# Kernel optimization log

Measured on AMD Instinct MI355X. Metric: run time of the kernel, lower is better.

Reference implementation:

```python
import math
import jax, jax.numpy as jnp
import numpy as np

LLM = 4096
QB = 512
SAM = 256
H = W = 64
OUT = 256
HEADS = 4
DH = SAM // HEADS
EPS = 1e-5


def _ln(x, g, b):
    mu = jnp.mean(x, axis=-1, keepdims=True)
    var = jnp.mean(jnp.square(x - mu), axis=-1, keepdims=True)
    return (x - mu) * jax.lax.rsqrt(var + EPS) * g + b


def _conv3x3(x, w):
    # x: (N,C,H,W), w: (O,I,3,3), padding=1
    return jax.lax.conv_general_dilated(
        x, w, window_strides=(1, 1), padding='SAME',
        dimension_numbers=('NCHW', 'OIHW', 'NCHW'))


def setup_inputs() -> dict:
    key = jax.random.key(0)
    ks = jax.random.split(key, 20)
    n = lambda k, sh, s: (jax.random.normal(k, sh, dtype=jnp.float32) * s)
    inp = {
        'image_embed': n(ks[0], (8, SAM, H, W), 1.0),
        'ref_vec': n(ks[1], (8, 32, LLM), 1.0),
        'querybook_slots': n(ks[2], (8, 32, QB), 1.0),
        # parameters (torch Linear layout: (out, in); conv: (O,I,kh,kw))
        'q_proj_w': n(ks[3], (HEADS * DH, LLM), 1.0 / math.sqrt(LLM)),
        'k_proj_w': n(ks[4], (HEADS * DH, SAM, 1, 1), 1.0 / math.sqrt(SAM)),
        'fuser_w1': n(ks[5], (HEADS, HEADS, 3, 3), 1.0 / math.sqrt(HEADS * 9)),
        'fuser_b1': n(ks[6], (HEADS,), 0.01),
        'fuser_w2': n(ks[7], (1, HEADS, 3, 3), 1.0 / math.sqrt(HEADS * 9)),
        'fuser_b2': jnp.full((1,), -1.8, dtype=jnp.float32),
        'qb_proj_w': n(ks[8], (LLM, QB), 1.0 / math.sqrt(QB)),
        'rf_ln_g': jnp.ones((2 * LLM,), jnp.float32),
        'rf_ln_b': jnp.zeros((2 * LLM,), jnp.float32),
        'rf_lin_w': n(ks[9], (LLM, 2 * LLM), 1.0 / math.sqrt(2 * LLM)),
        'rf_lin_b': n(ks[10], (LLM,), 0.01),
        'cf_ln_g': jnp.ones((LLM,), jnp.float32),
        'cf_ln_b': jnp.zeros((LLM,), jnp.float32),
        'cf_w1': n(ks[11], (LLM // 2, LLM), 1.0 / math.sqrt(LLM)),
        'cf_b1': n(ks[12], (LLM // 2,), 0.01),
        'cf_w2': n(ks[13], (1, LLM // 2), 1.0 / math.sqrt(LLM // 2)),
        'cf_b2': n(ks[14], (1,), 0.01),
    }
    return inp


def reference(image_embed, ref_vec, querybook_slots, q_proj_w, k_proj_w,
              fuser_w1, fuser_b1, fuser_w2, fuser_b2, qb_proj_w,
              rf_ln_g, rf_ln_b, rf_lin_w, rf_lin_b,
              cf_ln_g, cf_ln_b, cf_w1, cf_b1, cf_w2, cf_b2):
    B, C, h, w = image_embed.shape
    K = ref_vec.shape[1]
    # querybook projection + ref fuse
    qb = jnp.einsum('bkq,lq->bkl', querybook_slots, qb_proj_w)  # (B,K,LLM)
    cat = jnp.concatenate([ref_vec, qb], axis=-1)               # (B,K,2*LLM)
    fused = jax.nn.silu(jnp.einsum('bkc,lc->bkl', _ln(cat, rf_ln_g, rf_ln_b), rf_lin_w) + rf_lin_b)
    # per-slot query heads
    Q = jnp.einsum('bkl,ol->bko', fused, q_proj_w).reshape(B, K, HEADS, DH)
    # 1x1 conv key map -> (B,HEADS,DH,H,W)
    Kmap = jnp.einsum('bcxy,oc->boxy', image_embed, k_proj_w.reshape(HEADS * DH, SAM))
    Kmap = Kmap.reshape(B, HEADS, DH, h, w)
    # fused contraction over d_head (original materialized (B,K,HEADS,DH,H,W))
    logits_64_heads = jnp.einsum('bkhd,bhdxy->bkhxy', Q, Kmap) / math.sqrt(DH)
    x = logits_64_heads.reshape(B * K, HEADS, h, w)
    x = jax.nn.silu(_conv3x3(x, fuser_w1) + fuser_b1[None, :, None, None])
    logits_64 = _conv3x3(x, fuser_w2) + fuser_b2[None, :, None, None]  # (B*K,1,64,64)
    # bilinear upsample, align_corners=False (half-pixel centers)
    up = jax.image.resize(logits_64, (B * K, 1, OUT, OUT), method='bilinear')
    ref_logits_256 = up.reshape(B, K, OUT, OUT)
    # confidence head
    cfh = jax.nn.silu(jnp.einsum('bkl,ol->bko', _ln(fused, cf_ln_g, cf_ln_b), cf_w1) + cf_b1)
    conf_logits = (jnp.einsum('bko,lo->bkl', cfh, cf_w2) + cf_b2).squeeze(-1)  # (B,K)
    return ref_logits_256, conf_logits
```

## Files before the change

### kernel.cpp

```cpp
#include <hip/hip_runtime.h>

#define EPS 1e-5f

typedef __bf16 bf16_t;
typedef __bf16 bf16x8 __attribute__((ext_vector_type(8)));
typedef __bf16 bf16x4 __attribute__((ext_vector_type(4)));
typedef float f32x4 __attribute__((ext_vector_type(4)));

__device__ __forceinline__ float silu_f(float x) { return x / (1.f + __expf(-x)); }

__device__ __forceinline__ void gll16(const void* g, void* l) {
  __builtin_amdgcn_global_load_lds(
      (const __attribute__((address_space(1))) unsigned int*)g,
      (__attribute__((address_space(3))) unsigned int*)l, 16, 0, 0);
}

__device__ __forceinline__ float block_sum(float v, float* tmp) {
#pragma unroll
  for (int off = 32; off > 0; off >>= 1) v += __shfl_down(v, off);
  __syncthreads();
  if ((threadIdx.x & 63) == 0) tmp[threadIdx.x >> 6] = v;
  __syncthreads();
  return tmp[0] + tmp[1] + tmp[2] + tmp[3];
}

__global__ __launch_bounds__(1024) void gemm_gll(
    const bf16_t* __restrict__ A, const float* __restrict__ B,
    bf16_t* __restrict__ Cpart, int N, int K, int KS) {
  __shared__ bf16_t AsL[2][16384];
  __shared__ float BsL[2][8192];
  const int t = threadIdx.x;
  const int lane = t & 63;
  const int w = t >> 6;
  const int n0 = blockIdx.x * 128;
  const int kbeg = blockIdx.y * KS;
  const int nt = KS >> 6;

  const int arow0 = 16 * w + (lane >> 3);
  const int adch = (lane & 7) ^ (lane >> 3);
  const bf16_t* gA0 = A + (size_t)arow0 * K + kbeg + adch * 8;
  const bf16_t* gA1 = gA0 + (size_t)8 * K;
  const int brow0 = 8 * w + (lane >> 4);
  const int brow1 = brow0 + 4;
  const int bd0 = (lane & 15) ^ (brow0 & 15);
  const int bd1 = (lane & 15) ^ (brow1 & 15);
  const float* gB0 = B + (size_t)(n0 + brow0) * K + kbeg + bd0 * 4;
  const float* gB1 = B + (size_t)(n0 + brow1) * K + kbeg + bd1 * 4;

  f32x4 acc[4][2];
#pragma unroll
  for (int i = 0; i < 4; ++i)
#pragma unroll
    for (int j = 0; j < 2; ++j) acc[i][j] = f32x4{0.f, 0.f, 0.f, 0.f};

  const int wm = (w & 3) * 64;
  const int wn = (w >> 2) * 32;
  const int fr = lane & 15;
  const int kq = (lane >> 4) * 8;

  auto ISSUE = [&](int s, int p) {
    const int koff = s * 64;
    char* ab = (char*)&AsL[p][0] + 2 * w * 1024;
    char* bb = (char*)&BsL[p][0] + 2 * w * 1024;
    gll16(gA0 + koff, ab);
    gll16(gA1 + koff, ab + 1024);
    gll16(gB0 + koff, bb);
    gll16(gB1 + koff, bb + 1024);
  };

  auto COMPUTE = [&](int p) {
    const char* Ab = (const char*)&AsL[p][0];
    const char* Bb = (const char*)&BsL[p][0];
#pragma unroll
    for (int kk = 0; kk < 64; kk += 32) {
      const int col = kk + kq;
      bf16x8 af[4], bg[2];
#pragma unroll
      for (int i = 0; i < 4; ++i) {
        const int ra = wm + 16 * i + fr;
        const int sa = (col >> 3) ^ (ra & 7);
        af[i] = *(const bf16x8*)(Ab + ra * 128 + sa * 16);
      }
#pragma unroll
      for (int j = 0; j < 2; ++j) {
        const int rb = wn + 16 * j + fr;
        const int c0 = col >> 2;
        const int s0 = c0 ^ (rb & 15);
        const int s1 = (c0 + 1) ^ (rb & 15);
        f32x4 u0 = *(const f32x4*)(Bb + rb * 256 + s0 * 16);
        f32x4 u1 = *(const f32x4*)(Bb + rb * 256 + s1 * 16);
        bf16x8 bv;
        bv[0] = (bf16_t)u0[0]; bv[1] = (bf16_t)u0[1];
        bv[2] = (bf16_t)u0[2]; bv[3] = (bf16_t)u0[3];
        bv[4] = (bf16_t)u1[0]; bv[5] = (bf16_t)u1[1];
        bv[6] = (bf16_t)u1[2]; bv[7] = (bf16_t)u1[3];
        bg[j] = bv;
      }
#pragma unroll
      for (int i = 0; i < 4; ++i)
#pragma unroll
        for (int j = 0; j < 2; ++j)
          acc[i][j] = __builtin_amdgcn_mfma_f32_16x16x32_bf16(af[i], bg[j], acc[i][j], 0, 0, 0);
    }
  };

#define SB __builtin_amdgcn_sched_barrier(0);

  ISSUE(0, 0);
  if (nt > 1) ISSUE(1, 1);
  for (int s = 0; s < nt; ++s) {
    const int p = s & 1;
    if (s + 1 < nt) {
      asm volatile("s_waitcnt vmcnt(4)" ::: "memory");
    } else {
      asm volatile("s_waitcnt vmcnt(0)" ::: "memory");
    }
    SB __builtin_amdgcn_s_barrier(); SB
    COMPUTE(p);
    if (s + 2 < nt) {
      asm volatile("s_waitcnt lgkmcnt(0)" ::: "memory");
      SB __builtin_amdgcn_s_barrier(); SB
      ISSUE(s + 2, p);
    }
  }
#undef SB

  bf16_t* Cz = Cpart + (size_t)blockIdx.y * 256 * N;
  const int rh = (lane >> 4) * 4, col = lane & 15;
#pragma unroll
  for (int i = 0; i < 4; ++i)
#pragma unroll
    for (int j = 0; j < 2; ++j)
#pragma unroll
      for (int rr = 0; rr < 4; ++rr)
        Cz[(size_t)(wm + 16 * i + rh + rr) * N + n0 + wn + 16 * j + col] =
            (bf16_t)acc[i][j][rr];
}

__global__ __launch_bounds__(1024) void gemm_wide_s(
    const float* __restrict__ A, const float* __restrict__ B,
    bf16_t* __restrict__ Cpart, int N, int K, int KS) {
  __shared__ bf16_t As[256][72];
  __shared__ bf16_t Bs[128][72];
  const int t = threadIdx.x;
  const int lane = t & 63;
  const int w = t >> 6;
  const int n0 = blockIdx.x * 128;
  const int kbeg = blockIdx.y * KS;
  const int nt = KS >> 6;
  const int ar = t >> 2, ac = (t & 3) * 16;
  const int br = t >> 3, bc = (t & 7) * 8;
  const float* Ap = A + (size_t)ar * K + kbeg + ac;
  const float* Bp = B + (size_t)(n0 + br) * K + kbeg + bc;

  f32x4 acc[4][2];
#pragma unroll
  for (int i = 0; i < 4; ++i)
#pragma unroll
    for (int j = 0; j < 2; ++j) acc[i][j] = f32x4{0.f, 0.f, 0.f, 0.f};

  const int wm = (w & 3) * 64;
  const int wn = (w >> 2) * 32;
  const int fr = lane & 15;
  const int kq = (lane >> 4) * 8;

  for (int s = 0; s < nt; ++s) {
    float4 av[4], bv[2];
#pragma unroll
    for (int i = 0; i < 4; ++i) av[i] = *(const float4*)(Ap + s * 64 + 4 * i);
#pragma unroll
    for (int i = 0; i < 2; ++i) bv[i] = *(const float4*)(Bp + s * 64 + 4 * i);
    __syncthreads();
    {
      bf16x8 wa0, wa1, wb;
      wa0[0] = (bf16_t)av[0].x; wa0[1] = (bf16_t)av[0].y; wa0[2] = (bf16_t)av[0].z; wa0[3] = (bf16_t)av[0].w;
      wa0[4] = (bf16_t)av[1].x; wa0[5] = (bf16_t)av[1].y; wa0[6] = (bf16_t)av[1].z; wa0[7] = (bf16_t)av[1].w;
      wa1[0] = (bf16_t)av[2].x; wa1[1] = (bf16_t)av[2].y; wa1[2] = (bf16_t)av[2].z; wa1[3] = (bf16_t)av[2].w;
      wa1[4] = (bf16_t)av[3].x; wa1[5] = (bf16_t)av[3].y; wa1[6] = (bf16_t)av[3].z; wa1[7] = (bf16_t)av[3].w;
      wb[0] = (bf16_t)bv[0].x; wb[1] = (bf16_t)bv[0].y; wb[2] = (bf16_t)bv[0].z; wb[3] = (bf16_t)bv[0].w;
      wb[4] = (bf16_t)bv[1].x; wb[5] = (bf16_t)bv[1].y; wb[6] = (bf16_t)bv[1].z; wb[7] = (bf16_t)bv[1].w;
      *(bf16x8*)&As[ar][ac] = wa0;
      *(bf16x8*)&As[ar][ac + 8] = wa1;
      *(bf16x8*)&Bs[br][bc] = wb;
    }
    __syncthreads();
#pragma unroll
    for (int kk = 0; kk < 64; kk += 32) {
      bf16x8 af[4], bg[2];
#pragma unroll
      for (int i = 0; i < 4; ++i)
        af[i] = *(const bf16x8*)&As[wm + 16 * i + fr][kk + kq];
#pragma unroll
      for (int j = 0; j < 2; ++j)
        bg[j] = *(const bf16x8*)&Bs[wn + 16 * j + fr][kk + kq];
#pragma unroll
      for (int i = 0; i < 4; ++i)
#pragma unroll
        for (int j = 0; j < 2; ++j)
          acc[i][j] = __builtin_amdgcn_mfma_f32_16x16x32_bf16(af[i], bg[j], acc[i][j], 0, 0, 0);
    }
    __syncthreads();
  }

  bf16_t* Cz = Cpart + (size_t)blockIdx.y * 256 * N;
  const int rh = (lane >> 4) * 4, col = lane & 15;
#pragma unroll
  for (int i = 0; i < 4; ++i)
#pragma unroll
    for (int j = 0; j < 2; ++j)
#pragma unroll
      for (int rr = 0; rr < 4; ++rr)
        Cz[(size_t)(wm + 16 * i + rh + rr) * N + n0 + wn + 16 * j + col] =
            (bf16_t)acc[i][j][rr];
}

__global__ __launch_bounds__(256) void gemm_small(
    const bf16_t* __restrict__ A16, const float* __restrict__ B32, float* __restrict__ Cv,
    int M, int N, int K, int KS, int S) {
  __shared__ bf16_t As[64][72];
  __shared__ bf16_t Bs[64][72];
  const int t = threadIdx.x;
  const int lane = t & 63;
  const int w = t >> 6;
  const int s = blockIdx.z;
  const int n0 = blockIdx.x * 64;
  const int m0 = blockIdx.y * 64;
  const int kbeg = s * KS;

  f32x4 acc[2][2];
#pragma unroll
  for (int i = 0; i < 2; ++i)
#pragma unroll
    for (int j = 0; j < 2; ++j) acc[i][j] = f32x4{0.f, 0.f, 0.f, 0.f};

  const int wm = (w & 1) * 32, wn = (w >> 1) * 32;
  const int fr = lane & 15;
  const int kq = (lane >> 4) * 8;

  for (int k0 = kbeg; k0 < kbeg + KS; k0 += 64) {
    bf16x8 a8[2];
    float4 b4[4];
    {
      const int rr = t >> 2, c8 = (t & 3) * 8;
#pragma unroll
      for (int i = 0; i < 2; ++i)
        a8[i] = *(const bf16x8*)(A16 + (size_t)(m0 + rr) * K + k0 + c8 + 32 * i);
    }
    {
      const int rr = t >> 4, c4 = (t & 15) * 4;
#pragma unroll
      for (int i = 0; i < 4; ++i)
        b4[i] = *(const float4*)(B32 + (size_t)(n0 + rr + 16 * i) * K + k0 + c4);
    }
    __syncthreads();
    {
      const int rr = t >> 2, c8 = (t & 3) * 8;
#pragma unroll
      for (int i = 0; i < 2; ++i) *(bf16x8*)&As[rr][c8 + 32 * i] = a8[i];
    }
    {
      const int rr = t >> 4, c4 = (t & 15) * 4;
#pragma unroll
      for (int i = 0; i < 4; ++i) {
        bf16x4 v = {(bf16_t)b4[i].x, (bf16_t)b4[i].y, (bf16_t)b4[i].z, (bf16_t)b4[i].w};
        *(bf16x4*)&Bs[rr + 16 * i][c4] = v;
      }
    }
    __syncthreads();
#pragma unroll
    for (int kk = 0; kk < 64; kk += 32) {
      bf16x8 af[2], bg[2];
#pragma unroll
      for (int i = 0; i < 2; ++i) {
        af[i] = *(const bf16x8*)&As[wm + 16 * i + fr][kk + kq];
        bg[i] = *(const bf16x8*)&Bs[wn + 16 * i + fr][kk + kq];
      }
#pragma unroll
      for (int i = 0; i < 2; ++i)
#pragma unroll
        for (int j = 0; j < 2; ++j)
          acc[i][j] = __builtin_amdgcn_mfma_f32_16x16x32_bf16(af[i], bg[j], acc[i][j], 0, 0, 0);
    }
    __syncthreads();
  }

  const int rh = (lane >> 4) * 4;
  const int col = lane & 15;
#pragma unroll
  for (int i = 0; i < 2; ++i)
#pragma unroll
    for (int j = 0; j < 2; ++j)
#pragma unroll
      for (int rr = 0; rr < 4; ++rr)
        Cv[(size_t)s * M * N + (size_t)(m0 + wm + 16 * i + rh + rr) * N + n0 + wn + 16 * j + col] =
            acc[i][j][rr];
}

__global__ __launch_bounds__(512) void gemm_attn(
    const float* __restrict__ A, const float* __restrict__ B, bf16_t* __restrict__ C) {
  __shared__ bf16_t As[128][72];
  __shared__ bf16_t Bs[64][72];
  const int t = threadIdx.x;
  const int lane = t & 63;
  const int w = t >> 6;
  const int b = blockIdx.y;
  const int n0 = blockIdx.x * 64;
  const float* Ab = A + (size_t)b * 32768;
  const float* Bb = B + (size_t)b * 1048576;

  f32x4 acc[2][2];
#pragma unroll
  for (int i = 0; i < 2; ++i)
#pragma unroll
    for (int j = 0; j < 2; ++j) acc[i][j] = f32x4{0.f, 0.f, 0.f, 0.f};

  const int wm = (w & 3) * 32;
  const int wn = (w >> 2) * 32;
  const int fr = lane & 15;
  const int kq = (lane >> 4) * 8;

  for (int k0 = 0; k0 < 256; k0 += 64) {
    const int r = t >> 2, c4 = (t & 3) * 16;
    float4 a4[4];
#pragma unroll
    for (int i = 0; i < 4; ++i)
      a4[i] = *(const float4*)(Ab + (size_t)r * 256 + k0 + c4 + 4 * i);
    const int kr = t >> 3, nc = (t & 7) * 8;
    float4 b4[2];
#pragma unroll
    for (int i = 0; i < 2; ++i)
      b4[i] = *(const float4*)(Bb + (size_t)(k0 + kr) * 4096 + n0 + nc + 4 * i);
    __syncthreads();
#pragma unroll
    for (int i = 0; i < 4; ++i) {
      bf16x4 v = {(bf16_t)a4[i].x, (bf16_t)a4[i].y, (bf16_t)a4[i].z, (bf16_t)a4[i].w};
      *(bf16x4*)&As[r][c4 + 4 * i] = v;
    }
#pragma unroll
    for (int i = 0; i < 2; ++i) {
      Bs[nc + 4 * i + 0][kr] = (bf16_t)b4[i].x;
      Bs[nc + 4 * i + 1][kr] = (bf16_t)b4[i].y;
      Bs[nc + 4 * i + 2][kr] = (bf16_t)b4[i].z;
      Bs[nc + 4 * i + 3][kr] = (bf16_t)b4[i].w;
    }
    __syncthreads();
#pragma unroll
    for (int kk = 0; kk < 64; kk += 32) {
      bf16x8 af[2], bg[2];
#pragma unroll
      for (int i = 0; i < 2; ++i) {
        af[i] = *(const bf16x8*)&As[wm + 16 * i + fr][kk + kq];
        bg[i] = *(const bf16x8*)&Bs[wn + 16 * i + fr][kk + kq];
      }
#pragma unroll
      for (int i = 0; i < 2; ++i)
#pragma unroll
        for (int j = 0; j < 2; ++j)
          acc[i][j] = __builtin_amdgcn_mfma_f32_16x16x32_bf16(af[i], bg[j], acc[i][j], 0, 0, 0);
    }
    __syncthreads();
  }

  bf16_t* Cb = C + (size_t)b * 524288;
  const int rh = (lane >> 4) * 4, col = lane & 15;
#pragma unroll
  for (int i = 0; i < 2; ++i)
#pragma unroll
    for (int j = 0; j < 2; ++j)
#pragma unroll
      for (int rr = 0; rr < 4; ++rr)
        Cb[(size_t)(wm + 16 * i + rh + rr) * 4096 + n0 + wn + 16 * j + col] =
            (bf16_t)acc[i][j][rr];
}

__global__ __launch_bounds__(256) void red_ln(
    const bf16_t* __restrict__ partF, int S,
    const float* __restrict__ bias,
    const float* __restrict__ g, const float* __restrict__ bta,
    bf16_t* __restrict__ fusb, bf16_t* __restrict__ lnf) {
  __shared__ float tmp[4];
  const int row = blockIdx.x;
  const int t = threadIdx.x;
  const long i0 = t * 16;
  float a[16];
#pragma unroll
  for (int j = 0; j < 16; ++j) a[j] = 0.f;
  for (int s = 0; s < S; ++s) {
    const bf16_t* p = partF + (size_t)s * 1048576 + (size_t)row * 4096 + i0;
    bf16x8 v0 = *(const bf16x8*)(p);
    bf16x8 v1 = *(const bf16x8*)(p + 8);
#pragma unroll
    for (int j = 0; j < 8; ++j) { a[j] += (float)v0[j]; a[8 + j] += (float)v1[j]; }
  }
#pragma unroll
  for (int j = 0; j < 16; ++j) a[j] = silu_f(a[j] + bias[i0 + j]);
  {
    bf16x8 o0, o1;
#pragma unroll
    for (int j = 0; j < 8; ++j) { o0[j] = (bf16_t)a[j]; o1[j] = (bf16_t)a[8 + j]; }
    *(bf16x8*)(fusb + (size_t)row * 4096 + i0) = o0;
    *(bf16x8*)(fusb + (size_t)row * 4096 + i0 + 8) = o1;
  }
  float s1 = 0.f, s2 = 0.f;
#pragma unroll
  for (int j = 0; j < 16; ++j) { s1 += a[j]; s2 += a[j] * a[j]; }
  s1 = block_sum(s1, tmp);
  s2 = block_sum(s2, tmp);
  const float mu = s1 / 4096.f;
  const float inv = rsqrtf(s2 / 4096.f - mu * mu + EPS);
  bf16x8 o0, o1;
#pragma unroll
  for (int j = 0; j < 8; ++j) {
    o0[j] = (bf16_t)((a[j] - mu) * inv * g[i0 + j] + bta[i0 + j]);
    o1[j] = (bf16_t)((a[8 + j] - mu) * inv * g[i0 + 8 + j] + bta[i0 + 8 + j]);
  }
  *(bf16x8*)(lnf + (size_t)row * 4096 + i0) = o0;
  *(bf16x8*)(lnf + (size_t)row * 4096 + i0 + 8) = o1;
}

__global__ __launch_bounds__(256) void ln_fuse(
    const float* __restrict__ refv, const bf16_t* __restrict__ partQ, int S,
    const float* __restrict__ g, const float* __restrict__ bta, bf16_t* __restrict__ Y) {
  __shared__ float tmp[4];
  const int row = blockIdx.x;
  const int t = threadIdx.x;
  const long i0 = t * 16;
  float q[16];
#pragma unroll
  for (int j = 0; j < 16; ++j) q[j] = 0.f;
  for (int s = 0; s < S; ++s) {
    const bf16_t* p = partQ + (size_t)s * 1048576 + (size_t)row * 4096 + i0;
    bf16x8 v0 = *(const bf16x8*)(p);
    bf16x8 v1 = *(const bf16x8*)(p + 8);
#pragma unroll
    for (int j = 0; j < 8; ++j) { q[j] += (float)v0[j]; q[8 + j] += (float)v1[j]; }
  }
  const float* xr = refv + (size_t)row * 4096 + i0;
  float r[16];
#pragma unroll
  for (int j = 0; j < 4; ++j) {
    float4 v = *(const float4*)(xr + 4 * j);
    r[4 * j] = v.x; r[4 * j + 1] = v.y; r[4 * j + 2] = v.z; r[4 * j + 3] = v.w;
  }
  float s1 = 0.f, s2 = 0.f;
#pragma unroll
  for (int j = 0; j < 16; ++j) { s1 += r[j] + q[j]; s2 += r[j] * r[j] + q[j] * q[j]; }
  s1 = block_sum(s1, tmp);
  s2 = block_sum(s2, tmp);
  const float mu = s1 / 8192.f;
  const float inv = rsqrtf(s2 / 8192.f - mu * mu + EPS);
  bf16_t* y = Y + (size_t)row * 8192;
  bf16x8 o0, o1;
#pragma unroll
  for (int j = 0; j < 8; ++j) {
    o0[j] = (bf16_t)((r[j] - mu) * inv * g[i0 + j] + bta[i0 + j]);
    o1[j] = (bf16_t)((r[8 + j] - mu) * inv * g[i0 + 8 + j] + bta[i0 + 8 + j]);
  }
  *(bf16x8*)(y + i0) = o0;
  *(bf16x8*)(y + i0 + 8) = o1;
#pragma unroll
  for (int j = 0; j < 8; ++j) {
    o0[j] = (bf16_t)((q[j] - mu) * inv * g[4096 + i0 + j] + bta[4096 + i0 + j]);
    o1[j] = (bf16_t)((q[8 + j] - mu) * inv * g[4096 + i0 + 8 + j] + bta[4096 + i0 + 8 + j]);
  }
  *(bf16x8*)(y + 4096 + i0) = o0;
  *(bf16x8*)(y + 4096 + i0 + 8) = o1;
}

__global__ __launch_bounds__(256) void qw_fuse(
    const float* __restrict__ part8, const float* __restrict__ kW, float* __restrict__ QW) {
  __shared__ float q[256];
  const int bk = blockIdx.x;
  const int c = threadIdx.x;
  float sq = 0.f;
#pragma unroll
  for (int s = 0; s < 8; ++s) sq += part8[(size_t)s * 65536 + (size_t)bk * 256 + c];
  q[c] = 0.125f * sq;
  __syncthreads();
#pragma unroll
  for (int h = 0; h < 4; ++h) {
    float s = 0.f;
#pragma unroll 8
    for (int d = 0; d < 64; ++d)
      s += q[(h << 6) + d] * kW[(size_t)(((h << 6) + d) << 8) + c];
    QW[((size_t)(bk * 4 + h) << 8) + c] = s;
  }
}

__global__ __launch_bounds__(256) void conv_fused(
    const bf16_t* __restrict__ X, const float* __restrict__ W1,
    const float* __restrict__ B1, const float* __restrict__ W2,
    const float* __restrict__ B2, float* __restrict__ O) {
  __shared__ bf16_t lg[16384];
  __shared__ bf16_t mid[16384];
  __shared__ float lg64[4096];
  __shared__ float wsh[180];
  const int t = threadIdx.x;
  const size_t base = (size_t)blockIdx.x * 16384;
#pragma unroll
  for (int i = 0; i < 8; ++i) {
    int o = (i * 256 + t) * 8;
    *(bf16x8*)&lg[o] = *(const bf16x8*)(X + base + o);
  }
  if (t < 144) wsh[t] = W1[t];
  else if (t < 180) wsh[t] = W2[t - 144];
  __syncthreads();
  const int px0 = (t & 15) * 4, py0 = (t >> 4) * 4;
  {
    float acc1[4][16];
#pragma unroll
    for (int oc = 0; oc < 4; ++oc) {
      float bb = B1[oc];
#pragma unroll
      for (int p = 0; p < 16; ++p) acc1[oc][p] = bb;
    }
#pragma unroll
    for (int c = 0; c < 4; ++c) {
      float p[6][6];
#pragma unroll
      for (int yy = 0; yy < 6; ++yy) {
        int gy = py0 + yy - 1;
#pragma unroll
        for (int xx = 0; xx < 6; ++xx) {
          int gx = px0 + xx - 1;
          p[yy][xx] = ((unsigned)gy < 64u && (unsigned)gx < 64u)
                          ? (float)lg[c * 4096 + gy * 64 + gx] : 0.f;
        }
      }
#pragma unroll
      for (int oc = 0; oc < 4; ++oc) {
        float wr[9];
#pragma unroll
        for (int k = 0; k < 9; ++k) wr[k] = wsh[oc * 36 + c * 9 + k];
#pragma unroll
        for (int y = 0; y < 4; ++y)
#pragma unroll
          for (int x = 0; x < 4; ++x)
            acc1[oc][y * 4 + x] +=
                wr[0] * p[y][x] + wr[1] * p[y][x + 1] + wr[2] * p[y][x + 2]
              + wr[3] * p[y + 1][x] + wr[4] * p[y + 1][x + 1] + wr[5] * p[y + 1][x + 2]
              + wr[6] * p[y + 2][x] + wr[7] * p[y + 2][x + 1] + wr[8] * p[y + 2][x + 2];
      }
    }
#pragma unroll
    for (int oc = 0; oc < 4; ++oc)
#pragma unroll
      for (int y = 0; y < 4; ++y) {
        bf16x4 o;
#pragma unroll
        for (int x = 0; x < 4; ++x) o[x] = (bf16_t)silu_f(acc1[oc][y * 4 + x]);
        *(bf16x4*)&mid[oc * 4096 + (py0 + y) * 64 + px0] = o;
      }
  }
  __syncthreads();
  {
    float acc2[16];
    float bb = B2[0];
#pragma unroll
    for (int p = 0; p < 16; ++p) acc2[p] = bb;
#pragma unroll
    for (int c = 0; c < 4; ++c) {
      float p[6][6];
#pragma unroll
      for (int yy = 0; yy < 6; ++yy) {
        int gy = py0 + yy - 1;
#pragma unroll
        for (int xx = 0; xx < 6; ++xx) {
          int gx = px0 + xx - 1;
          p[yy][xx] = ((unsigned)gy < 64u && (unsigned)gx < 64u)
                          ? (float)mid[c * 4096 + gy * 64 + gx] : 0.f;
        }
      }
      float wr[9];
#pragma unroll
      for (int k = 0; k < 9; ++k) wr[k] = wsh[144 + c * 9 + k];
#pragma unroll
      for (int y = 0; y < 4; ++y)
#pragma unroll
        for (int x = 0; x < 4; ++x)
          acc2[y * 4 + x] +=
              wr[0] * p[y][x] + wr[1] * p[y][x + 1] + wr[2] * p[y][x + 2]
            + wr[3] * p[y + 1][x] + wr[4] * p[y + 1][x + 1] + wr[5] * p[y + 1][x + 2]
            + wr[6] * p[y + 2][x] + wr[7] * p[y + 2][x + 1] + wr[8] * p[y + 2][x + 2];
    }
#pragma unroll
    for (int y = 0; y < 4; ++y)
#pragma unroll
      for (int x = 0; x < 4; ++x) lg64[(py0 + y) * 64 + px0 + x] = acc2[y * 4 + x];
  }
  __syncthreads();
  float* Ob = O + (size_t)blockIdx.x * 65536;
  for (int rr = 0; rr < 64; ++rr) {
    int p4 = rr * 256 + t;
    int oy = p4 >> 6, ox0 = (p4 & 63) * 4;
    float sy = oy * 0.25f - 0.375f;
    int y0 = (int)floorf(sy);
    float wy = sy - (float)y0;
    int y1 = min(y0 + 1, 63); y0 = max(y0, 0);
    const float* r0 = &lg64[y0 * 64];
    const float* r1 = &lg64[y1 * 64];
    float4 o;
#pragma unroll
    for (int q = 0; q < 4; ++q) {
      int ox = ox0 + q;
      float sx = ox * 0.25f - 0.375f;
      int x0 = (int)floorf(sx);
      float wx = sx - (float)x0;
      int x1 = min(x0 + 1, 63); x0 = max(x0, 0);
      float v0 = r0[x0] + wx * (r0[x1] - r0[x0]);
      float v1 = r1[x0] + wx * (r1[x1] - r1[x0]);
      ((float*)&o)[q] = v0 + wy * (v1 - v0);
    }
    *(float4*)(Ob + oy * 256 + ox0) = o;
  }
}

__global__ __launch_bounds__(256) void conf_fuse(
    const bf16_t* __restrict__ partC, int S,
    const float* __restrict__ cb1, const float* __restrict__ w2,
    const float* __restrict__ b2, float* __restrict__ out) {
  __shared__ float tmp[4];
  const int row = blockIdx.x;
  const int t = threadIdx.x;
  const long i0 = t * 8;
  float a[8];
#pragma unroll
  for (int j = 0; j < 8; ++j) a[j] = 0.f;
  for (int s = 0; s < S; ++s) {
    bf16x8 v = *(const bf16x8*)(partC + (size_t)s * 524288 + (size_t)row * 2048 + i0);
#pragma unroll
    for (int j = 0; j < 8; ++j) a[j] += (float)v[j];
  }
  float dot = 0.f;
#pragma unroll
  for (int j = 0; j < 8; ++j) dot += silu_f(a[j] + cb1[i0 + j]) * w2[i0 + j];
  dot = block_sum(dot, tmp);
  if (t == 0) out[row] = dot + b2[0];
}

extern "C" void kernel_launch(void* const* d_in, const int* in_sizes, int n_in,
                              void* d_out, int out_size, void* d_ws, size_t ws_size,
                              hipStream_t stream) {
  const float* img    = (const float*)d_in[0];
  const float* refv   = (const float*)d_in[1];
  const float* qs     = (const float*)d_in[2];
  const float* qpw    = (const float*)d_in[3];
  const float* kpw    = (const float*)d_in[4];
  const float* fw1    = (const float*)d_in[5];
  const float* fb1    = (const float*)d_in[6];
  const float* fw2    = (const float*)d_in[7];
  const float* fb2    = (const float*)d_in[8];
  const float* qbw    = (const float*)d_in[9];
  const float* rlg    = (const float*)d_in[10];
  const float* rlb    = (const float*)d_in[11];
  const float* rlw    = (const float*)d_in[12];
  const float* rlbias = (const float*)d_in[13];
  const float* clg    = (const float*)d_in[14];
  const float* clb    = (const float*)d_in[15];
  const float* cw1    = (const float*)d_in[16];
  const float* cb1    = (const float*)d_in[17];
  const float* cw2    = (const float*)d_in[18];
  const float* cb2    = (const float*)d_in[19];
  float* out = (float*)d_out;
  char* W = (char*)d_ws;

  bf16_t* partQ = (bf16_t*)(W + 0);
  bf16_t* partF = (bf16_t*)(W + 0);
  bf16_t* l64hb = (bf16_t*)(W + 0);
  bf16_t* partC = (bf16_t*)(W + 0);
  bf16_t* catln = (bf16_t*)(W + 16777216);
  bf16_t* fusb  = (bf16_t*)(W + 20971520);
  bf16_t* lnf   = (bf16_t*)(W + 23068672);
  float*  part8 = (float*)(W + 25165824);
  float*  QW    = (float*)(W + 27262976);

  dim3 b256(256);

  gemm_wide_s<<<dim3(32, 8), dim3(1024), 0, stream>>>(qs, qbw, partQ, 4096, 512, 64);
  ln_fuse<<<dim3(256), b256, 0, stream>>>(refv, partQ, 8, rlg, rlb, catln);
  gemm_gll<<<dim3(32, 8), dim3(1024), 0, stream>>>(catln, rlw, partF, 4096, 8192, 1024);
  red_ln<<<dim3(256), b256, 0, stream>>>(partF, 8, rlbias, clg, clb, fusb, lnf);
  gemm_small<<<dim3(4, 4, 8), b256, 0, stream>>>(fusb, qpw, part8, 256, 256, 4096, 512, 8);
  qw_fuse<<<dim3(256), b256, 0, stream>>>(part8, kpw, QW);
  gemm_attn<<<dim3(64, 8), dim3(512), 0, stream>>>(QW, img, l64hb);
  conv_fused<<<dim3(256), b256, 0, stream>>>(l64hb, fw1, fb1, fw2, fb2, out);
  gemm_gll<<<dim3(16, 16), dim3(1024), 0, stream>>>(lnf, cw1, partC, 2048, 4096, 256);
  conf_fuse<<<dim3(256), b256, 0, stream>>>(partC, 16, cb1, cw2, cb2, out + 16777216);
}
```

Baseline: 178.0 us.

## Deepen gemm_gll pipeline to four stages with 32-wide K tiles

Restructures the gemm_gll kernel from a 2-buffer, 64-wide K pipeline into a 4-buffer ring with 32-wide K tiles, issuing three stages ahead. The second barrier after compute is gone because the next load goes into a buffer that is not in use. The XOR swizzle patterns and per-thread load addressing are rewritten for the narrower tiles. The aim is to hide global-load latency better and cut synchronisation. The trade-off is more loop iterations with less MFMA work per barrier. It also assumes nt is at least 3, since ISSUE(2,2) now runs unconditionally.

```diff
diff --git a/kernel.cpp b/kernel.cpp
--- a/kernel.cpp
+++ b/kernel.cpp
@@ -27,25 +27,21 @@
 __global__ __launch_bounds__(1024) void gemm_gll(
     const bf16_t* __restrict__ A, const float* __restrict__ B,
     bf16_t* __restrict__ Cpart, int N, int K, int KS) {
-  __shared__ bf16_t AsL[2][16384];
-  __shared__ float BsL[2][8192];
+  __shared__ bf16_t AsL[4][8192];
+  __shared__ float BsL[4][4096];
   const int t = threadIdx.x;
   const int lane = t & 63;
   const int w = t >> 6;
   const int n0 = blockIdx.x * 128;
   const int kbeg = blockIdx.y * KS;
-  const int nt = KS >> 6;
-
-  const int arow0 = 16 * w + (lane >> 3);
-  const int adch = (lane & 7) ^ (lane >> 3);
-  const bf16_t* gA0 = A + (size_t)arow0 * K + kbeg + adch * 8;
-  const bf16_t* gA1 = gA0 + (size_t)8 * K;
-  const int brow0 = 8 * w + (lane >> 4);
-  const int brow1 = brow0 + 4;
-  const int bd0 = (lane & 15) ^ (brow0 & 15);
-  const int bd1 = (lane & 15) ^ (brow1 & 15);
-  const float* gB0 = B + (size_t)(n0 + brow0) * K + kbeg + bd0 * 4;
-  const float* gB1 = B + (size_t)(n0 + brow1) * K + kbeg + bd1 * 4;
+  const int nt = KS >> 5;
+
+  const int arow = 16 * w + (lane >> 2);
+  const int adch = (lane & 3) ^ ((lane >> 2) & 3);
+  const bf16_t* gA = A + (size_t)arow * K + kbeg + adch * 8;
+  const int brow = 8 * w + (lane >> 3);
+  const int bdch = (lane & 7) ^ (lane >> 3);
+  const float* gB = B + (size_t)(n0 + brow) * K + kbeg + bdch * 4;
 
   f32x4 acc[4][2];
 #pragma unroll
@@ -56,72 +52,62 @@
   const int wm = (w & 3) * 64;
   const int wn = (w >> 2) * 32;
   const int fr = lane & 15;
-  const int kq = (lane >> 4) * 8;
+  const int kc = lane >> 4;
 
   auto ISSUE = [&](int s, int p) {
-    const int koff = s * 64;
-    char* ab = (char*)&AsL[p][0] + 2 * w * 1024;
-    char* bb = (char*)&BsL[p][0] + 2 * w * 1024;
-    gll16(gA0 + koff, ab);
-    gll16(gA1 + koff, ab + 1024);
-    gll16(gB0 + koff, bb);
-    gll16(gB1 + koff, bb + 1024);
+    const size_t koff = (size_t)s * 32;
+    gll16(gA + koff, (char*)&AsL[p][0] + w * 1024);
+    gll16(gB + koff, (char*)&BsL[p][0] + w * 1024);
   };
 
   auto COMPUTE = [&](int p) {
     const char* Ab = (const char*)&AsL[p][0];
     const char* Bb = (const char*)&BsL[p][0];
-#pragma unroll
-    for (int kk = 0; kk < 64; kk += 32) {
-      const int col = kk + kq;
-      bf16x8 af[4], bg[2];
-#pragma unroll
-      for (int i = 0; i < 4; ++i) {
-        const int ra = wm + 16 * i + fr;
-        const int sa = (col >> 3) ^ (ra & 7);
-        af[i] = *(const bf16x8*)(Ab + ra * 128 + sa * 16);
-      }
-#pragma unroll
-      for (int j = 0; j < 2; ++j) {
-        const int rb = wn + 16 * j + fr;
-        const int c0 = col >> 2;
-        const int s0 = c0 ^ (rb & 15);
-        const int s1 = (c0 + 1) ^ (rb & 15);
-        f32x4 u0 = *(const f32x4*)(Bb + rb * 256 + s0 * 16);
-        f32x4 u1 = *(const f32x4*)(Bb + rb * 256 + s1 * 16);
-        bf16x8 bv;
-        bv[0] = (bf16_t)u0[0]; bv[1] = (bf16_t)u0[1];
-        bv[2] = (bf16_t)u0[2]; bv[3] = (bf16_t)u0[3];
-        bv[4] = (bf16_t)u1[0]; bv[5] = (bf16_t)u1[1];
-        bv[6] = (bf16_t)u1[2]; bv[7] = (bf16_t)u1[3];
-        bg[j] = bv;
-      }
-#pragma unroll
-      for (int i = 0; i < 4; ++i)
-#pragma unroll
-        for (int j = 0; j < 2; ++j)
-          acc[i][j] = __builtin_amdgcn_mfma_f32_16x16x32_bf16(af[i], bg[j], acc[i][j], 0, 0, 0);
-    }
+    bf16x8 af[4], bg[2];
+#pragma unroll
+    for (int i = 0; i < 4; ++i) {
+      const int ra = wm + 16 * i + fr;
+      const int sa = kc ^ (ra & 3);
+      af[i] = *(const bf16x8*)(Ab + ra * 64 + sa * 16);
+    }
+#pragma unroll
+    for (int j = 0; j < 2; ++j) {
+      const int rb = wn + 16 * j + fr;
+      const int c0 = kc * 2;
+      const int s0 = c0 ^ (rb & 7);
+      const int s1 = (c0 + 1) ^ (rb & 7);
+      f32x4 u0 = *(const f32x4*)(Bb + rb * 128 + s0 * 16);
+      f32x4 u1 = *(const f32x4*)(Bb + rb * 128 + s1 * 16);
+      bf16x8 bv;
+      bv[0] = (bf16_t)u0[0]; bv[1] = (bf16_t)u0[1];
+      bv[2] = (bf16_t)u0[2]; bv[3] = (bf16_t)u0[3];
+      bv[4] = (bf16_t)u1[0]; bv[5] = (bf16_t)u1[1];
+      bv[6] = (bf16_t)u1[2]; bv[7] = (bf16_t)u1[3];
+      bg[j] = bv;
+    }
+#pragma unroll
+    for (int i = 0; i < 4; ++i)
+#pragma unroll
+      for (int j = 0; j < 2; ++j)
+        acc[i][j] = __builtin_amdgcn_mfma_f32_16x16x32_bf16(af[i], bg[j], acc[i][j], 0, 0, 0);
   };
 
 #define SB __builtin_amdgcn_sched_barrier(0);
 
   ISSUE(0, 0);
-  if (nt > 1) ISSUE(1, 1);
+  ISSUE(1, 1);
+  ISSUE(2, 2);
   for (int s = 0; s < nt; ++s) {
-    const int p = s & 1;
-    if (s + 1 < nt) {
+    if (s + 3 <= nt) {
       asm volatile("s_waitcnt vmcnt(4)" ::: "memory");
+    } else if (s + 2 == nt) {
+      asm volatile("s_waitcnt vmcnt(2)" ::: "memory");
     } else {
       asm volatile("s_waitcnt vmcnt(0)" ::: "memory");
     }
     SB __builtin_amdgcn_s_barrier(); SB
-    COMPUTE(p);
-    if (s + 2 < nt) {
-      asm volatile("s_waitcnt lgkmcnt(0)" ::: "memory");
-      SB __builtin_amdgcn_s_barrier(); SB
-      ISSUE(s + 2, p);
-    }
+    if (s + 3 < nt) ISSUE(s + 3, (s + 3) & 3);
+    COMPUTE(s & 3);
   }
 #undef SB
 
```

Measured after the change: 191.9 us. +7.8%, slower.

## Replace 1024-thread split-K GEMM with 256-thread 128x128 tile kernel, fewer K splits

Applied to the files above, without the earlier changes.

The large weight GEMMs now use a new 256-thread kernel with 128x128 output tiles split over M, N and K, where the old kernel computed the full 256-row M with 1024 threads. The K-split count drops (8 to 4 for the fusion GEMM and the query GEMM, 16 to 8 for the confidence GEMM), which reduces partial-sum traffic and reduction work. The explicit double-buffered global-to-LDS pipeline is dropped for a single buffer with __syncthreads, in exchange for more blocks per CU (launch bounds allow 3). The workspace offsets move to make room for the partial buffers.

```diff
diff --git a/kernel.cpp b/kernel.cpp
--- a/kernel.cpp
+++ b/kernel.cpp
@@ -24,71 +24,66 @@
   return tmp[0] + tmp[1] + tmp[2] + tmp[3];
 }
 
-__global__ __launch_bounds__(1024) void gemm_gll(
+__global__ __launch_bounds__(256, 3) void gemm_m97(
     const bf16_t* __restrict__ A, const float* __restrict__ B,
     bf16_t* __restrict__ Cpart, int N, int K, int KS) {
-  __shared__ bf16_t AsL[2][16384];
-  __shared__ float BsL[2][8192];
+  __shared__ bf16_t As[8192];
+  __shared__ float Bs[8192];
   const int t = threadIdx.x;
   const int lane = t & 63;
   const int w = t >> 6;
   const int n0 = blockIdx.x * 128;
-  const int kbeg = blockIdx.y * KS;
+  const int m0 = blockIdx.y * 128;
+  const int kbeg = blockIdx.z * KS;
   const int nt = KS >> 6;
 
-  const int arow0 = 16 * w + (lane >> 3);
-  const int adch = (lane & 7) ^ (lane >> 3);
-  const bf16_t* gA0 = A + (size_t)arow0 * K + kbeg + adch * 8;
-  const bf16_t* gA1 = gA0 + (size_t)8 * K;
-  const int brow0 = 8 * w + (lane >> 4);
-  const int brow1 = brow0 + 4;
-  const int bd0 = (lane & 15) ^ (brow0 & 15);
-  const int bd1 = (lane & 15) ^ (brow1 & 15);
-  const float* gB0 = B + (size_t)(n0 + brow0) * K + kbeg + bd0 * 4;
-  const float* gB1 = B + (size_t)(n0 + brow1) * K + kbeg + bd1 * 4;
-
-  f32x4 acc[4][2];
+  const int a_sub = lane >> 3;
+  const int adch = (lane & 7) ^ a_sub;
+  const bf16_t* gA = A + (size_t)(m0 + 32 * w + a_sub) * K + kbeg + adch * 8;
+  const int b_sub = lane >> 4;
+  const int blo = lane & 15;
+  const float* gB = B + (size_t)(n0 + 32 * w + b_sub) * K + kbeg;
+
+  f32x4 acc[4][4];
 #pragma unroll
   for (int i = 0; i < 4; ++i)
 #pragma unroll
-    for (int j = 0; j < 2; ++j) acc[i][j] = f32x4{0.f, 0.f, 0.f, 0.f};
-
-  const int wm = (w & 3) * 64;
-  const int wn = (w >> 2) * 32;
+    for (int j = 0; j < 4; ++j) acc[i][j] = f32x4{0.f, 0.f, 0.f, 0.f};
+
+  const int wm = (w & 1) * 64;
+  const int wn = (w >> 1) * 64;
   const int fr = lane & 15;
-  const int kq = (lane >> 4) * 8;
-
-  auto ISSUE = [&](int s, int p) {
-    const int koff = s * 64;
-    char* ab = (char*)&AsL[p][0] + 2 * w * 1024;
-    char* bb = (char*)&BsL[p][0] + 2 * w * 1024;
-    gll16(gA0 + koff, ab);
-    gll16(gA1 + koff, ab + 1024);
-    gll16(gB0 + koff, bb);
-    gll16(gB1 + koff, bb + 1024);
-  };
-
-  auto COMPUTE = [&](int p) {
-    const char* Ab = (const char*)&AsL[p][0];
-    const char* Bb = (const char*)&BsL[p][0];
+  const int kq8 = (lane >> 4) * 8;
+
+  for (int s = 0; s < nt; ++s) {
+#pragma unroll
+    for (int i = 0; i < 4; ++i)
+      gll16(gA + (size_t)(8 * i) * K + s * 64, (char*)As + (32 * w + 8 * i) * 128);
+#pragma unroll
+    for (int i = 0; i < 8; ++i) {
+      const int dch = blo ^ ((4 * i + b_sub) & 15);
+      gll16(gB + (size_t)(4 * i) * K + s * 64 + dch * 4,
+            (char*)Bs + (32 * w + 4 * i) * 256);
+    }
+    __syncthreads();
 #pragma unroll
     for (int kk = 0; kk < 64; kk += 32) {
-      const int col = kk + kq;
-      bf16x8 af[4], bg[2];
+      const int col = kk + kq8;
+      bf16x8 af[4], bg[4];
 #pragma unroll
       for (int i = 0; i < 4; ++i) {
         const int ra = wm + 16 * i + fr;
         const int sa = (col >> 3) ^ (ra & 7);
-        af[i] = *(const bf16x8*)(Ab + ra * 128 + sa * 16);
-      }
-#pragma unroll
-      for (int j = 0; j < 2; ++j) {
+        af[i] = *(const bf16x8*)((const char*)As + ra * 128 + sa * 16);
+      }
+#pragma unroll
+      for (int j = 0; j < 4; ++j) {
         const int rb = wn + 16 * j + fr;
         const int c0 = col >> 2;
         const int s0 = c0 ^ (rb & 15);
         const int s1 = (c0 + 1) ^ (rb & 15);
-        f32x4 u0 = *(const f32x4*)(Bb + rb * 256 + s0 * 16);
-        f32x4 u1 = *(const f32x4*)(Bb + rb * 256 + s1 * 16);
+        f32x4 u0 = *(const f32x4*)((const char*)Bs + rb * 256 + s0 * 16);
+        f32x4 u1 = *(const f32x4*)((const char*)Bs + rb * 256 + s1 * 16);
         bf16x8 bv;
         bv[0] = (bf16_t)u0[0]; bv[1] = (bf16_t)u0[1];
         bv[2] = (bf16_t)u0[2]; bv[3] = (bf16_t)u0[3];
@@ -99,41 +94,21 @@
 #pragma unroll
       for (int i = 0; i < 4; ++i)
 #pragma unroll
-        for (int j = 0; j < 2; ++j)
+        for (int j = 0; j < 4; ++j)
           acc[i][j] = __builtin_amdgcn_mfma_f32_16x16x32_bf16(af[i], bg[j], acc[i][j], 0, 0, 0);
     }
-  };
-
-#define SB __builtin_amdgcn_sched_barrier(0);
-
-  ISSUE(0, 0);
-  if (nt > 1) ISSUE(1, 1);
-  for (int s = 0; s < nt; ++s) {
-    const int p = s & 1;
-    if (s + 1 < nt) {
-      asm volatile("s_waitcnt vmcnt(4)" ::: "memory");
-    } else {
-      asm volatile("s_waitcnt vmcnt(0)" ::: "memory");
-    }
-    SB __builtin_amdgcn_s_barrier(); SB
-    COMPUTE(p);
-    if (s + 2 < nt) {
-      asm volatile("s_waitcnt lgkmcnt(0)" ::: "memory");
-      SB __builtin_amdgcn_s_barrier(); SB
-      ISSUE(s + 2, p);
-    }
-  }
-#undef SB
-
-  bf16_t* Cz = Cpart + (size_t)blockIdx.y * 256 * N;
+    __syncthreads();
+  }
+
+  bf16_t* Cz = Cpart + (size_t)blockIdx.z * 256 * N;
   const int rh = (lane >> 4) * 4, col = lane & 15;
 #pragma unroll
   for (int i = 0; i < 4; ++i)
 #pragma unroll
-    for (int j = 0; j < 2; ++j)
+    for (int j = 0; j < 4; ++j)
 #pragma unroll
       for (int rr = 0; rr < 4; ++rr)
-        Cz[(size_t)(wm + 16 * i + rh + rr) * N + n0 + wn + 16 * j + col] =
+        Cz[(size_t)(m0 + wm + 16 * i + rh + rr) * N + n0 + wn + 16 * j + col] =
             (bf16_t)acc[i][j][rr];
 }
 
@@ -668,22 +643,22 @@
   bf16_t* partF = (bf16_t*)(W + 0);
   bf16_t* l64hb = (bf16_t*)(W + 0);
   bf16_t* partC = (bf16_t*)(W + 0);
-  bf16_t* catln = (bf16_t*)(W + 16777216);
-  bf16_t* fusb  = (bf16_t*)(W + 20971520);
-  bf16_t* lnf   = (bf16_t*)(W + 23068672);
-  float*  part8 = (float*)(W + 25165824);
-  float*  QW    = (float*)(W + 27262976);
+  bf16_t* catln = (bf16_t*)(W + 33554432);
+  bf16_t* fusb  = (bf16_t*)(W + 37748736);
+  bf16_t* lnf   = (bf16_t*)(W + 39845888);
+  float*  part8 = (float*)(W + 41943040);
+  float*  QW    = (float*)(W + 44040192);
 
   dim3 b256(256);
 
-  gemm_wide_s<<<dim3(32, 8), dim3(1024), 0, stream>>>(qs, qbw, partQ, 4096, 512, 64);
-  ln_fuse<<<dim3(256), b256, 0, stream>>>(refv, partQ, 8, rlg, rlb, catln);
-  gemm_gll<<<dim3(32, 8), dim3(1024), 0, stream>>>(catln, rlw, partF, 4096, 8192, 1024);
-  red_ln<<<dim3(256), b256, 0, stream>>>(partF, 8, rlbias, clg, clb, fusb, lnf);
+  gemm_wide_s<<<dim3(32, 4), dim3(1024), 0, stream>>>(qs, qbw, partQ, 4096, 512, 128);
+  ln_fuse<<<dim3(256), b256, 0, stream>>>(refv, partQ, 4, rlg, rlb, catln);
+  gemm_m97<<<dim3(32, 2, 4), b256, 0, stream>>>(catln, rlw, partF, 4096, 8192, 2048);
+  red_ln<<<dim3(256), b256, 0, stream>>>(partF, 4, rlbias, clg, clb, fusb, lnf);
   gemm_small<<<dim3(4, 4, 8), b256, 0, stream>>>(fusb, qpw, part8, 256, 256, 4096, 512, 8);
   qw_fuse<<<dim3(256), b256, 0, stream>>>(part8, kpw, QW);
   gemm_attn<<<dim3(64, 8), dim3(512), 0, stream>>>(QW, img, l64hb);
   conv_fused<<<dim3(256), b256, 0, stream>>>(l64hb, fw1, fb1, fw2, fb2, out);
-  gemm_gll<<<dim3(16, 16), dim3(1024), 0, stream>>>(lnf, cw1, partC, 2048, 4096, 256);
-  conf_fuse<<<dim3(256), b256, 0, stream>>>(partC, 16, cb1, cw2, cb2, out + 16777216);
-}
+  gemm_m97<<<dim3(16, 2, 8), b256, 0, stream>>>(lnf, cw1, partC, 2048, 4096, 512);
+  conf_fuse<<<dim3(256), b256, 0, stream>>>(partC, 8, cb1, cw2, cb2, out + 16777216);
+}
```

New measurement: 184.4 us. +3.6%, slower.
